# Performance work log

Measured on AMD Instinct MI355X. Metric: run time of the kernel, lower is better.

Reference implementation:

```python
import jax, jax.numpy as jnp
import numpy as np
from math import factorial

# ---------------- real Wigner-3j (e3nn-style construction) ----------------

def _su2_cg(j1, j2, j3, m1, m2, m3):
    if m3 != m1 + m2 or not (abs(j1 - j2) <= j3 <= j1 + j2):
        return 0.0
    f = lambda n: float(factorial(n))
    pref = np.sqrt((2 * j3 + 1) * f(j1 + j2 - j3) * f(j1 - j2 + j3) * f(-j1 + j2 + j3) / f(j1 + j2 + j3 + 1))
    pref *= np.sqrt(f(j3 + m3) * f(j3 - m3) * f(j1 - m1) * f(j1 + m1) * f(j2 - m2) * f(j2 + m2))
    vmin = max(0, j2 - j3 - m1, j1 - j3 + m2)
    vmax = min(j1 + j2 - j3, j1 - m1, j2 + m2)
    s = 0.0
    for v in range(vmin, vmax + 1):
        s += (-1) ** v / (f(v) * f(j1 + j2 - j3 - v) * f(j1 - m1 - v) * f(j2 + m2 - v) * f(j3 - j2 + m1 + v) * f(j3 - j1 - m2 + v))
    return pref * s

def _q_real_to_complex(l):
    q = np.zeros((2 * l + 1, 2 * l + 1), dtype=complex)
    for m in range(-l, 0):
        q[l + m, l + abs(m)] = 1 / np.sqrt(2)
        q[l + m, l - abs(m)] = -1j / np.sqrt(2)
    q[l, l] = 1.0
    for m in range(1, l + 1):
        q[l + m, l + abs(m)] = (-1) ** m / np.sqrt(2)
        q[l + m, l - abs(m)] = 1j * (-1) ** m / np.sqrt(2)
    return (-1j) ** l * q

def real_wigner_3j(l1, l2, l3):
    Cc = np.zeros((2 * l1 + 1, 2 * l2 + 1, 2 * l3 + 1), dtype=complex)
    for i, m1 in enumerate(range(-l1, l1 + 1)):
        for j, m2 in enumerate(range(-l2, l2 + 1)):
            for k, m3 in enumerate(range(-l3, l3 + 1)):
                Cc[i, j, k] = _su2_cg(l1, l2, l3, m1, m2, m3)
    Q1, Q2, Q3 = _q_real_to_complex(l1), _q_real_to_complex(l2), _q_real_to_complex(l3)
    C = np.einsum('ia,jb,kc,ijk->abc', Q1, Q2, np.conj(Q3), Cc)
    Cr, Ci = np.real(C), np.imag(C)
    C = Cr if np.abs(Cr).sum() >= np.abs(Ci).sum() else Ci
    n = np.linalg.norm(C)
    return (C / n).astype(np.float32)

# ---------------- module constants ----------------
LMAX = 2
M_TOT = (LMAX + 1) ** 2          # 9
L_SLICES = {0: slice(0, 1), 1: slice(1, 4), 2: slice(4, 9)}
# uvu instruction paths (l1, l2=1, l3) with l3 <= LMAX, parity all even
PATHS = [(0, 1), (1, 0), (1, 1), (1, 2), (2, 1), (2, 2)]
# CG with 'component' irrep normalization: w3j * sqrt(2*l3+1)
W3J = {(l1, l3): real_wigner_3j(l1, 1, l3) * np.sqrt(2 * l3 + 1) for (l1, l3) in PATHS}
COEF1 = 2.04665350914            # E2TensorProduct_FirstOrder.get_coeffs()[1]
SH1_INT = float(np.sqrt(3.0 / (4.0 * np.pi)))  # l=1 'integral' normalization, normalize=False
# element path normalization: counts of paths landing on each output l (1x0e:1, 1e:3, 2e:2)
_counts = np.array([1.0] * 1 + [3.0] * 3 + [2.0] * 5, dtype=np.float32)
PATH_NORM = (1.0 / np.sqrt(_counts)).reshape(1, M_TOT, 1)

# ---------------- building blocks ----------------

def so3_linear(x, W, b):
    # per-degree equivariant linear: x [N, 9, Cin], W [3, Cin, Cout], b [Cout] (l=0 only)
    out = jnp.concatenate([jnp.einsum('nmc,cd->nmd', x[:, L_SLICES[l]], W[l]) for l in range(LMAX + 1)], axis=1)
    return out.at[:, 0, :].add(b)

def tp_uvu(x, y, tp_w):
    # depthwise (uvu) tensor product of x [N, 9, C] with l=1 vector y [N, 3]
    out = jnp.zeros_like(x)
    for p, (l1, l3) in enumerate(PATHS):
        C3 = jnp.asarray(W3J[(l1, l3)])  # [2l1+1, 3, 2l3+1]
        blk = jnp.einsum('abc,nau,nb->ncu', C3, x[:, L_SLICES[l1]], y)
        out = out.at[:, L_SLICES[l3]].add(blk * tp_w[p][None, None, :])
    return out

# ---------------- harness ----------------

def setup_inputs() -> dict:
    key = jax.random.key(0)
    ks = jax.random.split(key, 10)
    N1 = N2 = 4096; K = 16; H = 8; C = 128
    pos = jax.random.normal(ks[0], (N1, 3), dtype=jnp.float32)
    exp_pos = jax.random.normal(ks[1], (N2, 3), dtype=jnp.float32)
    h = jax.random.normal(ks[2], (N1, M_TOT, C), dtype=jnp.float32)
    exp_h = jax.random.normal(ks[3], (N2, M_TOT, C), dtype=jnp.float32)
    alpha_ij = jax.random.uniform(ks[4], (N1, K, H), dtype=jnp.float32)
    f_sparse_idx_expnode = jax.random.randint(ks[5], (N1, K), 0, N2)
    w1_w = jax.random.normal(ks[6], (LMAX + 1, C, C), dtype=jnp.float32) / np.sqrt(C)
    w1_b = jnp.zeros((C,), dtype=jnp.float32)
    w2_w = jax.random.normal(ks[7], (LMAX + 1, C, C), dtype=jnp.float32) / np.sqrt(C)
    w2_b = jnp.zeros((C,), dtype=jnp.float32)
    tp_w = jax.random.normal(ks[8], (len(PATHS), C), dtype=jnp.float32)
    return {"pos": pos, "exp_pos": exp_pos, "h": h, "exp_h": exp_h, "alpha_ij": alpha_ij,
            "f_sparse_idx_expnode": f_sparse_idx_expnode,
            "w1_w": w1_w, "w1_b": w1_b, "w2_w": w2_w, "w2_b": w2_b, "tp_w": tp_w}

def reference(pos, exp_pos, h, exp_h, alpha_ij, f_sparse_idx_expnode, w1_w, w1_b, w2_w, w2_b, tp_w):
    N1, K, H = alpha_ij.shape
    N2, M, C = exp_h.shape
    k = C // H
    exp_h1 = so3_linear(exp_h, w1_w, w1_b)            # w1 (simulated uvw mode)
    y1 = (COEF1 * SH1_INT) * pos                      # Y_powers[1] at target nodes, [N1,3]
    ey1 = (COEF1 * SH1_INT) * exp_pos                 # exp_Y_powers[1], [N2,3]
    # component 1: neighbor-aggregate features, then tensor product with Y(pos)
    gh = exp_h1.reshape(N2, M, H, k)[f_sparse_idx_expnode]          # [N1,K,M,H,k]
    c1 = jnp.einsum('bjh,bjmhk->bmhk', alpha_ij, gh).reshape(N1, M, C)
    c1 = tp_uvu(c1, y1, tp_w)                                       # [N1,M,C]
    # component 2: tensor product at source nodes with Y(exp_pos), then aggregate
    c2 = tp_uvu(exp_h1, ey1, tp_w)                                  # [N2,M,C]
    gc2 = c2.reshape(N2, M, H, k)[f_sparse_idx_expnode]             # [N1,K,M,H,k]
    c2 = jnp.einsum('bjh,bjmhk->bmhk', alpha_ij, gc2).reshape(N1, M, C)
    out = so3_linear(c1 - c2, w2_w, w2_b) * jnp.asarray(PATH_NORM)
    return out
```

## Files before the change

### kernel.cpp

```cpp
#include <hip/hip_runtime.h>

#define NN 4096
#define MTOT 9
#define CH 128

#define S3f 0.57735026918962576f
#define S2f 0.70710678118654752f
#define CUf 0.54772255750516611f
#define CVf 0.31622776601683794f
#define CWf 0.63245553203367587f
#define CAf 0.40824829046386302f
#define CA2f 0.81649658092772603f
#define YSf ((float)(2.04665350914 * 0.48860251190291992))

typedef __attribute__((ext_vector_type(8))) short short8;
typedef __attribute__((ext_vector_type(4))) float f32x4;
typedef __attribute__((ext_vector_type(2))) float f32x2;

__device__ __forceinline__ unsigned short f2b(float f) {
  unsigned u = __builtin_bit_cast(unsigned, f);
  u += 0x7FFFu + ((u >> 16) & 1u);
  return (unsigned short)(u >> 16);
}

__global__ __launch_bounds__(256) void wprep(
    const float* __restrict__ w1, const float* __restrict__ w2,
    unsigned short* __restrict__ o1, unsigned short* __restrict__ o2)
{
  int g = blockIdx.x * 256 + threadIdx.x;
  const float* W = w1;
  unsigned short* O = o1;
  int r = g;
  if (r >= 6144) { r -= 6144; W = w2; O = o2; }
  int l  = r >> 11;
  int r2 = r & 2047;
  int n  = r2 >> 4;
  int kq = r2 & 15;
  const float* src = W + l * 16384 + kq * 8 * CH + n;
  short8 v;
  #pragma unroll
  for (int j = 0; j < 8; ++j) v[j] = (short)f2b(src[j * CH]);
  *(short8*)(O + (size_t)l * 16384 + (((n >> 4) * 16 + kq) * 16 + (n & 15)) * 8) = v;
}

template <int XBF, int YBF, int NORM>
__global__ __launch_bounds__(256) void so3lin_mfma(
    const void* __restrict__ Xv, const unsigned short* __restrict__ Wsw,
    const float* __restrict__ bias, void* __restrict__ Yv)
{
  __shared__ unsigned short Bs[16384];
  const int bid = blockIdx.x;
  int l, blk0, m0, nm;
  if (bid < 64)       { l = 0; blk0 = bid;       m0 = 0; nm = 1; }
  else if (bid < 256) { l = 1; blk0 = bid - 64;  m0 = 1; nm = 3; }
  else                { l = 2; blk0 = bid - 256; m0 = 4; nm = 5; }
  const int t = threadIdx.x;

  {
    const float4* src = (const float4*)(Wsw + (size_t)l * 16384);
    float4* dst = (float4*)Bs;
    #pragma unroll
    for (int i = 0; i < 8; ++i) dst[t + i * 256] = src[t + i * 256];
  }
  __syncthreads();

  const int lane = t & 63;
  const int wave = t >> 6;
  const int c16  = lane & 15;
  const int quad = lane >> 4;
  const int rb   = (blk0 * 4 + wave) * 16;

  const int ra = rb + c16;
  const int nodeA = ra / nm;
  const int mA = m0 + (ra - nodeA * nm);
  const size_t abase = ((size_t)nodeA * MTOT + mA) * CH + quad * 8;

  f32x4 acc[8] = {};
  #pragma unroll
  for (int kk = 0; kk < CH; kk += 32) {
    short8 afrag;
    if (XBF) {
      afrag = *(const short8*)((const unsigned short*)Xv + abase + kk);
    } else {
      const float* xp = (const float*)Xv + abase + kk;
      float4 f0 = *(const float4*)xp;
      float4 f1 = *(const float4*)(xp + 4);
      afrag = (short8){(short)f2b(f0.x), (short)f2b(f0.y), (short)f2b(f0.z), (short)f2b(f0.w),
                       (short)f2b(f1.x), (short)f2b(f1.y), (short)f2b(f1.z), (short)f2b(f1.w)};
    }
    const int kq = (kk >> 3) + quad;
    #pragma unroll
    for (int ct = 0; ct < 8; ++ct) {
      short8 bfrag = *(const short8*)&Bs[((ct * 16 + kq) * 16 + c16) * 8];
      acc[ct] = __builtin_amdgcn_mfma_f32_16x16x32_bf16(afrag, bfrag, acc[ct], 0, 0, 0);
    }
  }

  const float scale = NORM ? (l == 0 ? 1.0f : (l == 1 ? S3f : S2f)) : 1.0f;
  #pragma unroll
  for (int i = 0; i < 4; ++i) {
    int r2 = rb + quad * 4 + i;
    int node2 = r2 / nm;
    int m2 = m0 + (r2 - node2 * nm);
    size_t obase = ((size_t)node2 * MTOT + m2) * CH + c16;
    #pragma unroll
    for (int ct = 0; ct < 8; ++ct) {
      float v = acc[ct][i];
      if (l == 0) v += bias[ct * 16 + c16];
      v *= scale;
      if (YBF) ((unsigned short*)Yv)[obase + ct * 16] = f2b(v);
      else     ((float*)Yv)[obase + ct * 16] = v;
    }
  }
}

#define PADK 136
__global__ __launch_bounds__(256) void agg_tp_w2(
    const unsigned short* __restrict__ X,
    const float* __restrict__ pos,
    const float* __restrict__ exp_pos,
    const float* __restrict__ alpha,
    const int*   __restrict__ idx,
    const float* __restrict__ tpw,
    const unsigned short* __restrict__ Wsw,
    const float* __restrict__ bias,
    float* __restrict__ out)
{
  __shared__ int   sIdx[4][16];
  __shared__ float sAl[4][128];
  __shared__ float sEy[4][48];
  __shared__ float sY[4][4];
  __shared__ __align__(16) unsigned short At[4 * 16 * PADK];
  const int t = threadIdx.x, wave = t >> 6, lane = t & 63;
  const int b = blockIdx.x * 4 + wave;

  if (lane < 16) sIdx[wave][lane] = idx[b * 16 + lane];
  sAl[wave][lane]      = alpha[b * 128 + lane];
  sAl[wave][lane + 64] = alpha[b * 128 + lane + 64];
  if (lane < 3) sY[wave][lane] = YSf * pos[b * 3 + lane];
  __syncthreads();
  if (lane < 48) {
    int j = lane / 3, cmp = lane - 3 * j;
    sEy[wave][lane] = YSf * exp_pos[sIdx[wave][j] * 3 + cmp];
  }
  __syncthreads();

  const int h = lane >> 3;
  const int c0 = lane * 2;
  f32x2 A0[9] = {}, A1[9] = {}, A2[9] = {}, A3[9] = {};
  #pragma unroll 2
  for (int j = 0; j < 16; ++j) {
    float al = sAl[wave][j * 8 + h];
    float e0 = al * sEy[wave][j * 3 + 0];
    float e1 = al * sEy[wave][j * 3 + 1];
    float e2 = al * sEy[wave][j * 3 + 2];
    f32x2 alv = {al, al};
    f32x2 e0v = {e0, e0};
    f32x2 e1v = {e1, e1};
    f32x2 e2v = {e2, e2};
    const unsigned short* xp = X + (size_t)sIdx[wave][j] * (MTOT * CH) + c0;
    #pragma unroll
    for (int m = 0; m < 9; ++m) {
      unsigned v = *(const unsigned*)(xp + m * CH);
      f32x2 x;
      x.x = __builtin_bit_cast(float, v << 16);
      x.y = __builtin_bit_cast(float, v & 0xFFFF0000u);
      A0[m] += alv * x; A1[m] += e0v * x; A2[m] += e1v * x; A3[m] += e2v * x;
    }
  }

  const float y0 = sY[wave][0], yv1 = sY[wave][1], y2 = sY[wave][2];
  float OUT[9][2];
  #pragma unroll
  for (int ch = 0; ch < 2; ++ch) {
    const int c = c0 + ch;
    const float w0 = tpw[c], w1 = tpw[CH + c], w2 = tpw[2 * CH + c];
    const float w3 = tpw[3 * CH + c], w4 = tpw[4 * CH + c], w5 = tpw[5 * CH + c];
    const float x0 = A0[0][ch];
    const float p0 = A0[1][ch], p1 = A0[2][ch], p2 = A0[3][ch];
    const float d0 = A0[4][ch], d1 = A0[5][ch], d2 = A0[6][ch], d3 = A0[7][ch], d4 = A0[8][ch];

    float r0 = w1 * S3f * (p0 * y0 + p1 * yv1 + p2 * y2);
    float r1 = w0 * x0 * y0 + w2 * S2f * (p1 * y2 - p2 * yv1)
             + w4 * (CUf * (d0 * y2 + d1 * yv1 - d4 * y0) - CVf * d2 * y0);
    float r2 = w0 * x0 * yv1 + w2 * S2f * (p2 * y0 - p0 * y2)
             + w4 * (CUf * (d1 * y0 + d3 * y2) + CWf * d2 * yv1);
    float r3 = w0 * x0 * y2 + w2 * S2f * (p0 * yv1 - p1 * y0)
             + w4 * (CUf * (d0 * y0 + d4 * y2 + d3 * yv1) - CVf * d2 * y2);
    float r4 = w3 * S2f * (p0 * y2 + p2 * y0)
             + w5 * (CAf * (d3 * y2 - d1 * y0) - 2.f * CAf * d4 * yv1);
    float r5 = w3 * S2f * (p0 * yv1 + p1 * y0)
             + w5 * (CAf * (d0 * y0 - d3 * yv1 + d4 * y2) + S2f * d2 * y2);
    float r6 = w3 * (CA2f * p1 * yv1 - CAf * (p0 * y0 + p2 * y2))
             + w5 * S2f * (d3 * y0 - d1 * y2);
    float r7 = w3 * S2f * (p1 * y2 + p2 * yv1)
             + w5 * (CAf * (d1 * yv1 - d0 * y2 + d4 * y0) - S2f * d2 * y0);
    float r8 = w3 * S2f * (p2 * y2 - p0 * y0)
             + w5 * CAf * (2.f * d0 * yv1 - d1 * y2 - d3 * y0);

    float q0 = w1 * S3f * (A1[1][ch] + A2[2][ch] + A3[3][ch]);
    float q1 = w0 * A1[0][ch] + w2 * S2f * (A3[2][ch] - A2[3][ch])
             + w4 * (CUf * (A3[4][ch] + A2[5][ch] - A1[8][ch]) - CVf * A1[6][ch]);
    float q2 = w0 * A2[0][ch] + w2 * S2f * (A1[3][ch] - A3[1][ch])
             + w4 * (CUf * (A1[5][ch] + A3[7][ch]) + CWf * A2[6][ch]);
    float q3 = w0 * A3[0][ch] + w2 * S2f * (A2[1][ch] - A1[2][ch])
             + w4 * (CUf * (A1[4][ch] + A3[8][ch] + A2[7][ch]) - CVf * A3[6][ch]);
    float q4 = w3 * S2f * (A3[1][ch] + A1[3][ch])
             + w5 * (CAf * (A3[7][ch] - A1[5][ch]) - 2.f * CAf * A2[8][ch]);
    float q5 = w3 * S2f * (A2[1][ch] + A1[2][ch])
             + w5 * (CAf * (A1[4][ch] - A2[7][ch] + A3[8][ch]) + S2f * A3[6][ch]);
    float q6 = w3 * (CA2f * A2[2][ch] - CAf * (A1[1][ch] + A3[3][ch]))
             + w5 * S2f * (A1[7][ch] - A3[5][ch]);
    float q7 = w3 * S2f * (A3[2][ch] + A2[3][ch])
             + w5 * (CAf * (A2[5][ch] - A3[4][ch] + A1[8][ch]) - S2f * A1[6][ch]);
    float q8 = w3 * S2f * (A3[3][ch] - A1[1][ch])
             + w5 * CAf * (2.f * A2[4][ch] - A3[5][ch] - A1[7][ch]);

    OUT[0][ch] = r0 - q0; OUT[1][ch] = r1 - q1; OUT[2][ch] = r2 - q2;
    OUT[3][ch] = r3 - q3; OUT[4][ch] = r4 - q4; OUT[5][ch] = r5 - q5;
    OUT[6][ch] = r6 - q6; OUT[7][ch] = r7 - q7; OUT[8][ch] = r8 - q8;
  }

  #pragma unroll
  for (int m = 0; m < 9; ++m) {
    int tt, rr;
    if (m == 0)      { tt = 0; rr = wave; }
    else if (m < 4)  { tt = 1; rr = wave * 3 + (m - 1); }
    else             { int g = wave * 5 + (m - 4); tt = 2 + (g >> 4); rr = g & 15; }
    unsigned dw = (unsigned)f2b(OUT[m][0]) | ((unsigned)f2b(OUT[m][1]) << 16);
    *(unsigned*)&At[(tt * 16 + rr) * PADK + c0] = dw;
  }
  __syncthreads();

  const int c16  = lane & 15;
  const int quad = lane >> 4;
  const int l2i  = (wave == 0) ? 0 : (wave == 1 ? 1 : 2);
  const unsigned short* Wl = Wsw + (size_t)l2i * 16384;

  f32x4 acc[8] = {};
  #pragma unroll
  for (int kk = 0; kk < CH; kk += 32) {
    short8 afrag = *(const short8*)&At[(wave * 16 + c16) * PADK + quad * 8 + kk];
    const int kq = (kk >> 3) + quad;
    #pragma unroll
    for (int ct = 0; ct < 8; ++ct) {
      short8 bfrag = *(const short8*)&Wl[((ct * 16 + kq) * 16 + c16) * 8];
      acc[ct] = __builtin_amdgcn_mfma_f32_16x16x32_bf16(afrag, bfrag, acc[ct], 0, 0, 0);
    }
  }

  const float scale = (wave == 0) ? 1.0f : (wave == 1 ? S3f : S2f);
  const int rmax = (wave == 1) ? 12 : ((wave == 2) ? 16 : 4);
  #pragma unroll
  for (int i = 0; i < 4; ++i) {
    int rr = quad * 4 + i;
    if (rr < rmax) {
      int node, m;
      if (wave == 0)      { node = rr; m = 0; }
      else if (wave == 1) { node = rr / 3; m = 1 + rr % 3; }
      else                { int g = (wave - 2) * 16 + rr; node = g / 5; m = 4 + g % 5; }
      size_t obase = ((size_t)(blockIdx.x * 4 + node) * MTOT + m) * CH + c16;
      #pragma unroll
      for (int ct = 0; ct < 8; ++ct) {
        float v = acc[ct][i];
        if (wave == 0) v += bias[ct * 16 + c16];
        out[obase + ct * 16] = v * scale;
      }
    }
  }
}

extern "C" void kernel_launch(void* const* d_in, const int* in_sizes, int n_in,
                              void* d_out, int out_size, void* d_ws, size_t ws_size,
                              hipStream_t stream) {
  (void)in_sizes; (void)n_in; (void)out_size; (void)ws_size;
  const float* pos     = (const float*)d_in[0];
  const float* exp_pos = (const float*)d_in[1];
  const float* exp_h   = (const float*)d_in[3];
  const float* alpha   = (const float*)d_in[4];
  const int*   idx     = (const int*)d_in[5];
  const float* w1w     = (const float*)d_in[6];
  const float* w1b     = (const float*)d_in[7];
  const float* w2w     = (const float*)d_in[8];
  const float* w2b     = (const float*)d_in[9];
  const float* tpw     = (const float*)d_in[10];
  float* out = (float*)d_out;

  unsigned short* eh1 = (unsigned short*)d_ws;
  unsigned short* w1s = eh1 + (size_t)NN * MTOT * CH;
  unsigned short* w2s = w1s + 3 * 16384;

  wprep<<<48, 256, 0, stream>>>(w1w, w2w, w1s, w2s);
  so3lin_mfma<0, 1, 0><<<576, 256, 0, stream>>>(exp_h, w1s, w1b, eh1);
  agg_tp_w2<<<NN / 4, 256, 0, stream>>>(eh1, pos, exp_pos, alpha, idx, tpw, w2s, w2b, out);
}
```

Before: 139.4 us.

## Store intermediate features channel-pair-major and batch gather loads in aggregation

The first linear kernel now writes its bf16 output in a transposed layout, where each channel pair keeps all 9 m-components together in 48 contiguous bytes. The aggregation kernel can then fetch a neighbor's features with two 16-byte loads and one 4-byte load per lane, instead of nine scattered 4-byte loads. It also issues loads for 4 neighbors ahead of the FMA work to expose more memory-level parallelism. The cost is scattered 2-byte stores in the producer kernel and higher register pressure in the consumer.

Result: slower. 154.7 us (+11.0%).

```diff
diff --git a/kernel.cpp b/kernel.cpp
--- a/kernel.cpp
+++ b/kernel.cpp
@@ -43,7 +43,7 @@
   *(short8*)(O + (size_t)l * 16384 + (((n >> 4) * 16 + kq) * 16 + (n & 15)) * 8) = v;
 }
 
-template <int XBF, int YBF, int NORM>
+template <int XBF, int YT, int NORM>
 __global__ __launch_bounds__(256) void so3lin_mfma(
     const void* __restrict__ Xv, const unsigned short* __restrict__ Wsw,
     const float* __restrict__ bias, void* __restrict__ Yv)
@@ -102,14 +102,17 @@
     int r2 = rb + quad * 4 + i;
     int node2 = r2 / nm;
     int m2 = m0 + (r2 - node2 * nm);
-    size_t obase = ((size_t)node2 * MTOT + m2) * CH + c16;
     #pragma unroll
     for (int ct = 0; ct < 8; ++ct) {
       float v = acc[ct][i];
       if (l == 0) v += bias[ct * 16 + c16];
       v *= scale;
-      if (YBF) ((unsigned short*)Yv)[obase + ct * 16] = f2b(v);
-      else     ((float*)Yv)[obase + ct * 16] = v;
+      if (YT) {
+        int c = ct * 16 + c16;
+        ((unsigned short*)Yv)[(size_t)node2 * 1536 + (c >> 1) * 24 + m2 * 2 + (c & 1)] = f2b(v);
+      } else {
+        ((float*)Yv)[((size_t)node2 * MTOT + m2) * CH + c16 + ct * 16] = v;
+      }
     }
   }
 }
@@ -148,24 +151,38 @@
   const int h = lane >> 3;
   const int c0 = lane * 2;
   f32x2 A0[9] = {}, A1[9] = {}, A2[9] = {}, A3[9] = {};
-  #pragma unroll 2
-  for (int j = 0; j < 16; ++j) {
-    float al = sAl[wave][j * 8 + h];
-    float e0 = al * sEy[wave][j * 3 + 0];
-    float e1 = al * sEy[wave][j * 3 + 1];
-    float e2 = al * sEy[wave][j * 3 + 2];
-    f32x2 alv = {al, al};
-    f32x2 e0v = {e0, e0};
-    f32x2 e1v = {e1, e1};
-    f32x2 e2v = {e2, e2};
-    const unsigned short* xp = X + (size_t)sIdx[wave][j] * (MTOT * CH) + c0;
-    #pragma unroll
-    for (int m = 0; m < 9; ++m) {
-      unsigned v = *(const unsigned*)(xp + m * CH);
-      f32x2 x;
-      x.x = __builtin_bit_cast(float, v << 16);
-      x.y = __builtin_bit_cast(float, v & 0xFFFF0000u);
-      A0[m] += alv * x; A1[m] += e0v * x; A2[m] += e1v * x; A3[m] += e2v * x;
+  for (int jb = 0; jb < 16; jb += 4) {
+    uint4 qa[4], qb[4]; unsigned qc[4];
+    #pragma unroll
+    for (int jj = 0; jj < 4; ++jj) {
+      const char* src = (const char*)X + (size_t)sIdx[wave][jb + jj] * 3072 + lane * 48;
+      qa[jj] = *(const uint4*)(src);
+      qb[jj] = *(const uint4*)(src + 16);
+      qc[jj] = *(const unsigned*)(src + 32);
+    }
+    #pragma unroll
+    for (int jj = 0; jj < 4; ++jj) {
+      const int j = jb + jj;
+      float al = sAl[wave][j * 8 + h];
+      float e0 = al * sEy[wave][j * 3 + 0];
+      float e1 = al * sEy[wave][j * 3 + 1];
+      float e2 = al * sEy[wave][j * 3 + 2];
+      f32x2 alv = {al, al};
+      f32x2 e0v = {e0, e0};
+      f32x2 e1v = {e1, e1};
+      f32x2 e2v = {e2, e2};
+      unsigned vv[9];
+      vv[0] = qa[jj].x; vv[1] = qa[jj].y; vv[2] = qa[jj].z; vv[3] = qa[jj].w;
+      vv[4] = qb[jj].x; vv[5] = qb[jj].y; vv[6] = qb[jj].z; vv[7] = qb[jj].w;
+      vv[8] = qc[jj];
+      #pragma unroll
+      for (int m = 0; m < 9; ++m) {
+        unsigned v = vv[m];
+        f32x2 x;
+        x.x = __builtin_bit_cast(float, v << 16);
+        x.y = __builtin_bit_cast(float, v & 0xFFFF0000u);
+        A0[m] += alv * x; A1[m] += e0v * x; A2[m] += e1v * x; A3[m] += e2v * x;
+      }
     }
   }
 
@@ -286,11 +303,11 @@
   const float* tpw     = (const float*)d_in[10];
   float* out = (float*)d_out;
 
-  unsigned short* eh1 = (unsigned short*)d_ws;
-  unsigned short* w1s = eh1 + (size_t)NN * MTOT * CH;
-  unsigned short* w2s = w1s + 3 * 16384;
+  unsigned short* eh1T = (unsigned short*)d_ws;
+  unsigned short* w1s  = eh1T + (size_t)NN * 1536;
+  unsigned short* w2s  = w1s + 3 * 16384;
 
   wprep<<<48, 256, 0, stream>>>(w1w, w2w, w1s, w2s);
-  so3lin_mfma<0, 1, 0><<<576, 256, 0, stream>>>(exp_h, w1s, w1b, eh1);
-  agg_tp_w2<<<NN / 4, 256, 0, stream>>>(eh1, pos, exp_pos, alpha, idx, tpw, w2s, w2b, out);
-}
+  so3lin_mfma<0, 1, 0><<<576, 256, 0, stream>>>(exp_h, w1s, w1b, eh1T);
+  agg_tp_w2<<<NN / 4, 256, 0, stream>>>(eh1T, pos, exp_pos, alpha, idx, tpw, w2s, w2b, out);
+}
```

## Split neighbor aggregation across two wave halves with LDS reduction in agg_tp_w2

Applied to the files above, without the earlier changes.

Doubles the block to 512 threads so each of the four target nodes gets two waves. Each wave gathers half of the 16 neighbors, and the partial moments are reduced through shared memory in two phases. The w2 MFMA stage is also split so each wave computes half of the output column tiles. This targets the latency of the dependent gather loop and raises parallelism per node. In exchange it adds extra barriers, LDS traffic (40KB shared buffer, which may limit occupancy) and more idle lanes during the tensor-product stage.

New measurement: 150.6 us. 8.1% more time.

```diff
diff --git a/kernel.cpp b/kernel.cpp
--- a/kernel.cpp
+++ b/kernel.cpp
@@ -115,7 +115,7 @@
 }
 
 #define PADK 136
-__global__ __launch_bounds__(256) void agg_tp_w2(
+__global__ __launch_bounds__(512) void agg_tp_w2(
     const unsigned short* __restrict__ X,
     const float* __restrict__ pos,
     const float* __restrict__ exp_pos,
@@ -130,18 +130,24 @@
   __shared__ float sAl[4][128];
   __shared__ float sEy[4][48];
   __shared__ float sY[4][4];
-  __shared__ __align__(16) unsigned short At[4 * 16 * PADK];
+  __shared__ __align__(16) char UU[40960];
+  float* mom = (float*)UU;
+  unsigned short* At = (unsigned short*)UU;
+
   const int t = threadIdx.x, wave = t >> 6, lane = t & 63;
-  const int b = blockIdx.x * 4 + wave;
-
-  if (lane < 16) sIdx[wave][lane] = idx[b * 16 + lane];
-  sAl[wave][lane]      = alpha[b * 128 + lane];
-  sAl[wave][lane + 64] = alpha[b * 128 + lane + 64];
-  if (lane < 3) sY[wave][lane] = YSf * pos[b * 3 + lane];
+  const int n4 = wave & 3, half = wave >> 2;
+  const int b = blockIdx.x * 4 + n4;
+
+  if (half == 0) {
+    if (lane < 16) sIdx[n4][lane] = idx[b * 16 + lane];
+    sAl[n4][lane]      = alpha[b * 128 + lane];
+    sAl[n4][lane + 64] = alpha[b * 128 + lane + 64];
+    if (lane < 3) sY[n4][lane] = YSf * pos[b * 3 + lane];
+  }
   __syncthreads();
-  if (lane < 48) {
+  if (half == 0 && lane < 48) {
     int j = lane / 3, cmp = lane - 3 * j;
-    sEy[wave][lane] = YSf * exp_pos[sIdx[wave][j] * 3 + cmp];
+    sEy[n4][lane] = YSf * exp_pos[sIdx[n4][j] * 3 + cmp];
   }
   __syncthreads();
 
@@ -149,16 +155,17 @@
   const int c0 = lane * 2;
   f32x2 A0[9] = {}, A1[9] = {}, A2[9] = {}, A3[9] = {};
   #pragma unroll 2
-  for (int j = 0; j < 16; ++j) {
-    float al = sAl[wave][j * 8 + h];
-    float e0 = al * sEy[wave][j * 3 + 0];
-    float e1 = al * sEy[wave][j * 3 + 1];
-    float e2 = al * sEy[wave][j * 3 + 2];
+  for (int jj = 0; jj < 8; ++jj) {
+    const int j = half * 8 + jj;
+    float al = sAl[n4][j * 8 + h];
+    float e0 = al * sEy[n4][j * 3 + 0];
+    float e1 = al * sEy[n4][j * 3 + 1];
+    float e2 = al * sEy[n4][j * 3 + 2];
     f32x2 alv = {al, al};
     f32x2 e0v = {e0, e0};
     f32x2 e1v = {e1, e1};
     f32x2 e2v = {e2, e2};
-    const unsigned short* xp = X + (size_t)sIdx[wave][j] * (MTOT * CH) + c0;
+    const unsigned short* xp = X + (size_t)sIdx[n4][j] * (MTOT * CH) + c0;
     #pragma unroll
     for (int m = 0; m < 9; ++m) {
       unsigned v = *(const unsigned*)(xp + m * CH);
@@ -169,102 +176,132 @@
     }
   }
 
-  const float y0 = sY[wave][0], yv1 = sY[wave][1], y2 = sY[wave][2];
-  float OUT[9][2];
-  #pragma unroll
-  for (int ch = 0; ch < 2; ++ch) {
-    const int c = c0 + ch;
-    const float w0 = tpw[c], w1 = tpw[CH + c], w2 = tpw[2 * CH + c];
-    const float w3 = tpw[3 * CH + c], w4 = tpw[4 * CH + c], w5 = tpw[5 * CH + c];
-    const float x0 = A0[0][ch];
-    const float p0 = A0[1][ch], p1 = A0[2][ch], p2 = A0[3][ch];
-    const float d0 = A0[4][ch], d1 = A0[5][ch], d2 = A0[6][ch], d3 = A0[7][ch], d4 = A0[8][ch];
-
-    float r0 = w1 * S3f * (p0 * y0 + p1 * yv1 + p2 * y2);
-    float r1 = w0 * x0 * y0 + w2 * S2f * (p1 * y2 - p2 * yv1)
-             + w4 * (CUf * (d0 * y2 + d1 * yv1 - d4 * y0) - CVf * d2 * y0);
-    float r2 = w0 * x0 * yv1 + w2 * S2f * (p2 * y0 - p0 * y2)
-             + w4 * (CUf * (d1 * y0 + d3 * y2) + CWf * d2 * yv1);
-    float r3 = w0 * x0 * y2 + w2 * S2f * (p0 * yv1 - p1 * y0)
-             + w4 * (CUf * (d0 * y0 + d4 * y2 + d3 * yv1) - CVf * d2 * y2);
-    float r4 = w3 * S2f * (p0 * y2 + p2 * y0)
-             + w5 * (CAf * (d3 * y2 - d1 * y0) - 2.f * CAf * d4 * yv1);
-    float r5 = w3 * S2f * (p0 * yv1 + p1 * y0)
-             + w5 * (CAf * (d0 * y0 - d3 * yv1 + d4 * y2) + S2f * d2 * y2);
-    float r6 = w3 * (CA2f * p1 * yv1 - CAf * (p0 * y0 + p2 * y2))
-             + w5 * S2f * (d3 * y0 - d1 * y2);
-    float r7 = w3 * S2f * (p1 * y2 + p2 * yv1)
-             + w5 * (CAf * (d1 * yv1 - d0 * y2 + d4 * y0) - S2f * d2 * y0);
-    float r8 = w3 * S2f * (p2 * y2 - p0 * y0)
-             + w5 * CAf * (2.f * d0 * yv1 - d1 * y2 - d3 * y0);
-
-    float q0 = w1 * S3f * (A1[1][ch] + A2[2][ch] + A3[3][ch]);
-    float q1 = w0 * A1[0][ch] + w2 * S2f * (A3[2][ch] - A2[3][ch])
-             + w4 * (CUf * (A3[4][ch] + A2[5][ch] - A1[8][ch]) - CVf * A1[6][ch]);
-    float q2 = w0 * A2[0][ch] + w2 * S2f * (A1[3][ch] - A3[1][ch])
-             + w4 * (CUf * (A1[5][ch] + A3[7][ch]) + CWf * A2[6][ch]);
-    float q3 = w0 * A3[0][ch] + w2 * S2f * (A2[1][ch] - A1[2][ch])
-             + w4 * (CUf * (A1[4][ch] + A3[8][ch] + A2[7][ch]) - CVf * A3[6][ch]);
-    float q4 = w3 * S2f * (A3[1][ch] + A1[3][ch])
-             + w5 * (CAf * (A3[7][ch] - A1[5][ch]) - 2.f * CAf * A2[8][ch]);
-    float q5 = w3 * S2f * (A2[1][ch] + A1[2][ch])
-             + w5 * (CAf * (A1[4][ch] - A2[7][ch] + A3[8][ch]) + S2f * A3[6][ch]);
-    float q6 = w3 * (CA2f * A2[2][ch] - CAf * (A1[1][ch] + A3[3][ch]))
-             + w5 * S2f * (A1[7][ch] - A3[5][ch]);
-    float q7 = w3 * S2f * (A3[2][ch] + A2[3][ch])
-             + w5 * (CAf * (A2[5][ch] - A3[4][ch] + A1[8][ch]) - S2f * A1[6][ch]);
-    float q8 = w3 * S2f * (A3[3][ch] - A1[1][ch])
-             + w5 * CAf * (2.f * A2[4][ch] - A3[5][ch] - A1[7][ch]);
-
-    OUT[0][ch] = r0 - q0; OUT[1][ch] = r1 - q1; OUT[2][ch] = r2 - q2;
-    OUT[3][ch] = r3 - q3; OUT[4][ch] = r4 - q4; OUT[5][ch] = r5 - q5;
-    OUT[6][ch] = r6 - q6; OUT[7][ch] = r7 - q7; OUT[8][ch] = r8 - q8;
-  }
-
-  #pragma unroll
-  for (int m = 0; m < 9; ++m) {
-    int tt, rr;
-    if (m == 0)      { tt = 0; rr = wave; }
-    else if (m < 4)  { tt = 1; rr = wave * 3 + (m - 1); }
-    else             { int g = wave * 5 + (m - 4); tt = 2 + (g >> 4); rr = g & 15; }
-    unsigned dw = (unsigned)f2b(OUT[m][0]) | ((unsigned)f2b(OUT[m][1]) << 16);
-    *(unsigned*)&At[(tt * 16 + rr) * PADK + c0] = dw;
+  #pragma unroll
+  for (int ph = 0; ph < 2; ++ph) {
+    const int m0p = ph ? 5 : 0;
+    const int nmp = ph ? 4 : 5;
+    if (half == 1) {
+      #pragma unroll
+      for (int dm = 0; dm < nmp; ++dm) {
+        *(f32x2*)&mom[2 * ((((n4 * 4 + 0) * 5) + dm) * 64 + lane)] = A0[m0p + dm];
+        *(f32x2*)&mom[2 * ((((n4 * 4 + 1) * 5) + dm) * 64 + lane)] = A1[m0p + dm];
+        *(f32x2*)&mom[2 * ((((n4 * 4 + 2) * 5) + dm) * 64 + lane)] = A2[m0p + dm];
+        *(f32x2*)&mom[2 * ((((n4 * 4 + 3) * 5) + dm) * 64 + lane)] = A3[m0p + dm];
+      }
+    }
+    __syncthreads();
+    if (half == 0) {
+      #pragma unroll
+      for (int dm = 0; dm < nmp; ++dm) {
+        A0[m0p + dm] += *(const f32x2*)&mom[2 * ((((n4 * 4 + 0) * 5) + dm) * 64 + lane)];
+        A1[m0p + dm] += *(const f32x2*)&mom[2 * ((((n4 * 4 + 1) * 5) + dm) * 64 + lane)];
+        A2[m0p + dm] += *(const f32x2*)&mom[2 * ((((n4 * 4 + 2) * 5) + dm) * 64 + lane)];
+        A3[m0p + dm] += *(const f32x2*)&mom[2 * ((((n4 * 4 + 3) * 5) + dm) * 64 + lane)];
+      }
+    }
+    __syncthreads();
+  }
+
+  if (half == 0) {
+    const float y0 = sY[n4][0], yv1 = sY[n4][1], y2 = sY[n4][2];
+    float OUT[9][2];
+    #pragma unroll
+    for (int ch = 0; ch < 2; ++ch) {
+      const int c = c0 + ch;
+      const float w0 = tpw[c], w1 = tpw[CH + c], w2 = tpw[2 * CH + c];
+      const float w3 = tpw[3 * CH + c], w4 = tpw[4 * CH + c], w5 = tpw[5 * CH + c];
+      const float x0 = A0[0][ch];
+      const float p0 = A0[1][ch], p1 = A0[2][ch], p2 = A0[3][ch];
+      const float d0 = A0[4][ch], d1 = A0[5][ch], d2 = A0[6][ch], d3 = A0[7][ch], d4 = A0[8][ch];
+
+      float r0 = w1 * S3f * (p0 * y0 + p1 * yv1 + p2 * y2);
+      float r1 = w0 * x0 * y0 + w2 * S2f * (p1 * y2 - p2 * yv1)
+               + w4 * (CUf * (d0 * y2 + d1 * yv1 - d4 * y0) - CVf * d2 * y0);
+      float r2 = w0 * x0 * yv1 + w2 * S2f * (p2 * y0 - p0 * y2)
+               + w4 * (CUf * (d1 * y0 + d3 * y2) + CWf * d2 * yv1);
+      float r3 = w0 * x0 * y2 + w2 * S2f * (p0 * yv1 - p1 * y0)
+               + w4 * (CUf * (d0 * y0 + d4 * y2 + d3 * yv1) - CVf * d2 * y2);
+      float r4 = w3 * S2f * (p0 * y2 + p2 * y0)
+               + w5 * (CAf * (d3 * y2 - d1 * y0) - 2.f * CAf * d4 * yv1);
+      float r5 = w3 * S2f * (p0 * yv1 + p1 * y0)
+               + w5 * (CAf * (d0 * y0 - d3 * yv1 + d4 * y2) + S2f * d2 * y2);
+      float r6 = w3 * (CA2f * p1 * yv1 - CAf * (p0 * y0 + p2 * y2))
+               + w5 * S2f * (d3 * y0 - d1 * y2);
+      float r7 = w3 * S2f * (p1 * y2 + p2 * yv1)
+               + w5 * (CAf * (d1 * yv1 - d0 * y2 + d4 * y0) - S2f * d2 * y0);
+      float r8 = w3 * S2f * (p2 * y2 - p0 * y0)
+               + w5 * CAf * (2.f * d0 * yv1 - d1 * y2 - d3 * y0);
+
+      float q0 = w1 * S3f * (A1[1][ch] + A2[2][ch] + A3[3][ch]);
+      float q1 = w0 * A1[0][ch] + w2 * S2f * (A3[2][ch] - A2[3][ch])
+               + w4 * (CUf * (A3[4][ch] + A2[5][ch] - A1[8][ch]) - CVf * A1[6][ch]);
+      float q2 = w0 * A2[0][ch] + w2 * S2f * (A1[3][ch] - A3[1][ch])
+               + w4 * (CUf * (A1[5][ch] + A3[7][ch]) + CWf * A2[6][ch]);
+      float q3 = w0 * A3[0][ch] + w2 * S2f * (A2[1][ch] - A1[2][ch])
+               + w4 * (CUf * (A1[4][ch] + A3[8][ch] + A2[7][ch]) - CVf * A3[6][ch]);
+      float q4 = w3 * S2f * (A3[1][ch] + A1[3][ch])
+               + w5 * (CAf * (A3[7][ch] - A1[5][ch]) - 2.f * CAf * A2[8][ch]);
+      float q5 = w3 * S2f * (A2[1][ch] + A1[2][ch])
+               + w5 * (CAf * (A1[4][ch] - A2[7][ch] + A3[8][ch]) + S2f * A3[6][ch]);
+      float q6 = w3 * (CA2f * A2[2][ch] - CAf * (A1[1][ch] + A3[3][ch]))
+               + w5 * S2f * (A1[7][ch] - A3[5][ch]);
+      float q7 = w3 * S2f * (A3[2][ch] + A2[3][ch])
+               + w5 * (CAf * (A2[5][ch] - A3[4][ch] + A1[8][ch]) - S2f * A1[6][ch]);
+      float q8 = w3 * S2f * (A3[3][ch] - A1[1][ch])
+               + w5 * CAf * (2.f * A2[4][ch] - A3[5][ch] - A1[7][ch]);
+
+      OUT[0][ch] = r0 - q0; OUT[1][ch] = r1 - q1; OUT[2][ch] = r2 - q2;
+      OUT[3][ch] = r3 - q3; OUT[4][ch] = r4 - q4; OUT[5][ch] = r5 - q5;
+      OUT[6][ch] = r6 - q6; OUT[7][ch] = r7 - q7; OUT[8][ch] = r8 - q8;
+    }
+
+    #pragma unroll
+    for (int m = 0; m < 9; ++m) {
+      int tt, rr;
+      if (m == 0)      { tt = 0; rr = n4; }
+      else if (m < 4)  { tt = 1; rr = n4 * 3 + (m - 1); }
+      else             { int g = n4 * 5 + (m - 4); tt = 2 + (g >> 4); rr = g & 15; }
+      unsigned dw = (unsigned)f2b(OUT[m][0]) | ((unsigned)f2b(OUT[m][1]) << 16);
+      *(unsigned*)&At[(tt * 16 + rr) * PADK + c0] = dw;
+    }
   }
   __syncthreads();
 
   const int c16  = lane & 15;
   const int quad = lane >> 4;
-  const int l2i  = (wave == 0) ? 0 : (wave == 1 ? 1 : 2);
+  const int tw   = wave & 3;
+  const int ctb  = half * 4;
+  const int l2i  = (tw == 0) ? 0 : (tw == 1 ? 1 : 2);
   const unsigned short* Wl = Wsw + (size_t)l2i * 16384;
 
-  f32x4 acc[8] = {};
+  f32x4 acc[4] = {};
   #pragma unroll
   for (int kk = 0; kk < CH; kk += 32) {
-    short8 afrag = *(const short8*)&At[(wave * 16 + c16) * PADK + quad * 8 + kk];
+    short8 afrag = *(const short8*)&At[(tw * 16 + c16) * PADK + quad * 8 + kk];
     const int kq = (kk >> 3) + quad;
     #pragma unroll
-    for (int ct = 0; ct < 8; ++ct) {
-      short8 bfrag = *(const short8*)&Wl[((ct * 16 + kq) * 16 + c16) * 8];
+    for (int ct = 0; ct < 4; ++ct) {
+      short8 bfrag = *(const short8*)&Wl[(((ctb + ct) * 16 + kq) * 16 + c16) * 8];
       acc[ct] = __builtin_amdgcn_mfma_f32_16x16x32_bf16(afrag, bfrag, acc[ct], 0, 0, 0);
     }
   }
 
-  const float scale = (wave == 0) ? 1.0f : (wave == 1 ? S3f : S2f);
-  const int rmax = (wave == 1) ? 12 : ((wave == 2) ? 16 : 4);
+  const float scale = (tw == 0) ? 1.0f : (tw == 1 ? S3f : S2f);
+  const int rmax = (tw == 1) ? 12 : ((tw == 2) ? 16 : 4);
   #pragma unroll
   for (int i = 0; i < 4; ++i) {
     int rr = quad * 4 + i;
     if (rr < rmax) {
       int node, m;
-      if (wave == 0)      { node = rr; m = 0; }
-      else if (wave == 1) { node = rr / 3; m = 1 + rr % 3; }
-      else                { int g = (wave - 2) * 16 + rr; node = g / 5; m = 4 + g % 5; }
+      if (tw == 0)      { node = rr; m = 0; }
+      else if (tw == 1) { node = rr / 3; m = 1 + rr % 3; }
+      else              { int g = (tw - 2) * 16 + rr; node = g / 5; m = 4 + g % 5; }
       size_t obase = ((size_t)(blockIdx.x * 4 + node) * MTOT + m) * CH + c16;
       #pragma unroll
-      for (int ct = 0; ct < 8; ++ct) {
+      for (int ct = 0; ct < 4; ++ct) {
         float v = acc[ct][i];
-        if (wave == 0) v += bias[ct * 16 + c16];
-        out[obase + ct * 16] = v * scale;
+        if (tw == 0) v += bias[(ctb + ct) * 16 + c16];
+        out[obase + (ctb + ct) * 16] = v * scale;
       }
     }
   }
@@ -292,5 +329,5 @@
 
   wprep<<<48, 256, 0, stream>>>(w1w, w2w, w1s, w2s);
   so3lin_mfma<0, 1, 0><<<576, 256, 0, stream>>>(exp_h, w1s, w1b, eh1);
-  agg_tp_w2<<<NN / 4, 256, 0, stream>>>(eh1, pos, exp_pos, alpha, idx, tpw, w2s, w2b, out);
-}
+  agg_tp_w2<<<NN / 4, 512, 0, stream>>>(eh1, pos, exp_pos, alpha, idx, tpw, w2s, w2b, out);
+}
```
